# Optimization experiments

Hardware: AMD Instinct MI355X
Metric: run time of the kernel (lower is better)

Reference implementation:

```python
import jax, jax.numpy as jnp
import numpy as np

B = 8192
DIM = 1024
NI = 16
ALPHA = 0.5
BETA = 1.0


def setup_inputs() -> dict:
    key = jax.random.key(0)
    ks = jax.random.split(key, 12)
    d, n = DIM, NI
    din = d + d // n  # local expert input width = 1088
    s = 0.02  # small init scale to keep softplus in a sane range
    return {
        "y": jax.random.normal(ks[0], (B, d), jnp.float32),
        "M": jax.random.normal(ks[1], (B, d), jnp.float32),
        # global discriminator params ([in, out] layout)
        "gw0": jax.random.normal(ks[2], (d, d), jnp.float32) * s,
        "gb0": jnp.zeros((d,), jnp.float32),
        "gw1": jax.random.normal(ks[3], (d, d), jnp.float32) * s,
        "gb1": jnp.zeros((d,), jnp.float32),
        "l0w": jax.random.normal(ks[4], (2 * d, 128), jnp.float32) * s,
        "l0b": jnp.zeros((128,), jnp.float32),
        "l1w": jax.random.normal(ks[5], (128, 128), jnp.float32) * s,
        "l1b": jnp.zeros((128,), jnp.float32),
        "l2w": jax.random.normal(ks[6], (128, 1), jnp.float32) * s,
        "l2b": jnp.zeros((1,), jnp.float32),
        # local discriminator: n_interpretator stacked expert MLPs
        "lW1": jax.random.normal(ks[7], (n, din, 128), jnp.float32) * s,
        "lb1": jnp.zeros((n, 128), jnp.float32),
        "lW2": jax.random.normal(ks[8], (n, 128, 128), jnp.float32) * s,
        "lb2": jnp.zeros((n, 128), jnp.float32),
        "lW3": jax.random.normal(ks[9], (n, 128, 1), jnp.float32) * s,
        "lb3": jnp.zeros((n, 1), jnp.float32),
        "n_interpretator": NI,
    }


def reference(y, M, gw0, gb0, gw1, gb1, l0w, l0b, l1w, l1b, l2w, l2b,
              lW1, lb1, lW2, lb2, lW3, lb3, n_interpretator):
    n = n_interpretator
    Bsz, d = y.shape
    M3 = M.reshape(Bsz, d // n, n)                              # [B, d/n, n]
    Mp3 = jnp.concatenate([M3[1:], M3[:1]], axis=0)             # shuffled negatives
    y_exp = jnp.broadcast_to(y[:, :, None], (Bsz, d, n))        # [B, d, n]
    yM = jnp.concatenate([M3, y_exp], axis=1)                   # [B, d/n + d, n]
    yMp = jnp.concatenate([Mp3, y_exp], axis=1)

    def local_d(x):
        # batched over the n expert groups: grouped GEMMs instead of a loop
        h = jax.nn.relu(jnp.einsum('bdn,ndh->bnh', x, lW1) + lb1)   # [B, n, 128]
        h = jax.nn.relu(jnp.einsum('bnh,nhk->bnk', h, lW2) + lb2)   # [B, n, 128]
        s = jnp.einsum('bnh,nho->bno', h, lW3) + lb3                # [B, n, 1]
        return s[..., 0]                                            # [B, n]

    Ej_l = -jnp.mean(jax.nn.softplus(-local_d(yM)))
    Em_l = jnp.mean(jax.nn.softplus(local_d(yMp)))
    LOCAL = (Em_l - Ej_l) * BETA

    def global_d(yy, Mm):
        h = jax.nn.relu(Mm.reshape(Bsz, -1) @ gw0 + gb0) @ gw1 + gb1  # net(M)
        h = jnp.concatenate([yy, h], axis=1)                          # [B, 2d]
        h = jax.nn.relu(h @ l0w + l0b)
        h = jax.nn.relu(h @ l1w + l1b)
        return h @ l2w + l2b                                          # [B, 1]

    Ej_g = -jnp.mean(jax.nn.softplus(-global_d(y, M3)))
    Em_g = jnp.mean(jax.nn.softplus(global_d(y, Mp3)))
    GLOBAL = (Em_g - Ej_g) * ALPHA

    return LOCAL + GLOBAL
```

## Files before the change

kernel.cpp:

```cpp
#include <hip/hip_runtime.h>
#include <hip/hip_bf16.h>
#include <math.h>

#define B_ROWS 8192
#define NEXP 16

typedef __attribute__((ext_vector_type(8))) short short8;
typedef __attribute__((ext_vector_type(4))) float f32x4;

__device__ __forceinline__ float softplus_f(float x) {
    return fmaxf(x, 0.f) + log1pf(expf(-fabsf(x)));
}

__device__ __forceinline__ float bf2f(short u) {
    union { unsigned int i; float f; } c;
    c.i = ((unsigned int)(unsigned short)u) << 16;
    return c.f;
}

__device__ __forceinline__ short f2bf_s(float x) {
    __hip_bfloat16 h = __float2bfloat16(x);
    return *(short*)&h;
}

__device__ __forceinline__ void gll16(const void* g, void* l) {
    __builtin_amdgcn_global_load_lds(
        (const __attribute__((address_space(1))) void*)g,
        (__attribute__((address_space(3))) void*)l, 16, 0, 0);
}

#define FENCE() asm volatile("" ::: "memory")
#define VM3 asm volatile("s_waitcnt vmcnt(3)" ::: "memory")
#define VM0 asm volatile("s_waitcnt vmcnt(0)" ::: "memory")
#define BAR __builtin_amdgcn_s_barrier()

__global__ __launch_bounds__(256) void prep_all(
    const float* __restrict__ y, const float* __restrict__ M,
    const float* __restrict__ lW1, const float* __restrict__ gw0,
    const float* __restrict__ l0w, const float* __restrict__ gb1,
    const float* __restrict__ l0b, const float* __restrict__ lW2,
    const float* __restrict__ l1w, const float* __restrict__ gw1,
    __hip_bfloat16* __restrict__ yb, short* __restrict__ Mt2,
    __hip_bfloat16* __restrict__ W1yt, short* __restrict__ W1m2,
    __hip_bfloat16* __restrict__ W0p, __hip_bfloat16* __restrict__ l0wyt,
    float* __restrict__ bing, short* __restrict__ W2sb,
    short* __restrict__ L1ws, float* __restrict__ wgtp,
    double* __restrict__ acc, int* __restrict__ counter)
{
    __shared__ __align__(16) char smem[33280];
    const int b = blockIdx.x;
    const int tid = threadIdx.x;
    const int lane = tid & 63, w = tid >> 6;

    if (b < 64) {
        short* As = (short*)smem;
        short* Bs = (short*)(smem + 16384);
        const int ct = b & 7, ks = b >> 3;
        const int bn = ct * 128;
        const int wr = w >> 1, wc = w & 1;
        const int l15 = lane & 15, l4 = lane >> 4;

        f32x4 acc4[4][4] = {};
        for (int kq = 0; kq < 2; ++kq) {
            const int k0 = ks * 128 + kq * 64;
            {
                int c4 = (tid & 31) * 4;
                int kkr0 = tid >> 5;
                #pragma unroll
                for (int r = 0; r < 8; ++r) {
                    int kk = r * 8 + kkr0;
                    float4 v = *(const float4*)&l0w[(long)(1024 + k0 + kk) * 128 + c4];
                    int g = kk >> 3, sub = kk & 7;
                    #pragma unroll
                    for (int i = 0; i < 4; ++i) {
                        int row = c4 + i;
                        As[row * 64 + (g ^ (row & 7)) * 8 + sub] = f2bf_s(((const float*)&v)[i]);
                    }
                }
            }
            {
                int jr0 = tid >> 3;
                int g = tid & 7;
                #pragma unroll
                for (int s = 0; s < 4; ++s) {
                    int jrel = s * 32 + jr0;
                    const float* src = &gw1[(long)(bn + jrel) * 1024 + k0 + g * 8];
                    float4 v0 = *(const float4*)src;
                    float4 v1 = *(const float4*)(src + 4);
                    union { short8 v; short sh[8]; } o;
                    o.sh[0] = f2bf_s(v0.x); o.sh[1] = f2bf_s(v0.y);
                    o.sh[2] = f2bf_s(v0.z); o.sh[3] = f2bf_s(v0.w);
                    o.sh[4] = f2bf_s(v1.x); o.sh[5] = f2bf_s(v1.y);
                    o.sh[6] = f2bf_s(v1.z); o.sh[7] = f2bf_s(v1.w);
                    *(short8*)&Bs[jrel * 64 + (g ^ (jrel & 7)) * 8] = o.v;
                }
            }
            __syncthreads();
            #pragma unroll
            for (int st = 0; st < 2; ++st) {
                const int gr = (st * 4 + l4) ^ (l15 & 7);
                short8 a[4], bv[4];
                #pragma unroll
                for (int m = 0; m < 4; ++m)
                    a[m] = *(const short8*)&As[(wr * 64 + m * 16 + l15) * 64 + gr * 8];
                #pragma unroll
                for (int n = 0; n < 4; ++n)
                    bv[n] = *(const short8*)&Bs[(wc * 64 + n * 16 + l15) * 64 + gr * 8];
                #pragma unroll
                for (int m = 0; m < 4; ++m)
                    #pragma unroll
                    for (int n = 0; n < 4; ++n)
                        acc4[m][n] = __builtin_amdgcn_mfma_f32_16x16x32_bf16(a[m], bv[n], acc4[m][n], 0, 0, 0);
            }
            __syncthreads();
        }
        #pragma unroll
        for (int m = 0; m < 4; ++m) {
            int row = wr * 64 + m * 16 + l4 * 4;
            #pragma unroll
            for (int n = 0; n < 4; ++n) {
                int col = bn + wc * 64 + n * 16 + l15;
                #pragma unroll
                for (int r = 0; r < 4; ++r)
                    wgtp[((long)ks * 128 + row + r) * 1024 + col] = acc4[m][n][r];
            }
        }
        return;
    }

    if (b == 64) {
        float* part = (float*)smem;
        const int c = tid & 127, h2 = tid >> 7;
        float s = h2 ? 0.f : l0b[c];
        const float* p = l0w + (long)(1024 + h2 * 512) * 128 + c;
        const float* g = gb1 + h2 * 512;
        #pragma unroll 8
        for (int o = 0; o < 512; ++o)
            s = fmaf(g[o], p[(long)o * 128], s);
        part[tid] = s;
        __syncthreads();
        if (tid < 128) bing[tid] = part[tid] + part[tid + 128];
        if (tid == 255) { acc[0] = 0.0; acc[1] = 0.0; *counter = 0; }
        return;
    }

    if (b < 1089) {
        const long base = (long)(b - 65) * 2048;
        #pragma unroll
        for (int j = 0; j < 8; ++j) {
            long i = base + j * 256 + tid;
            float4 v = ((const float4*)y)[i];
            union { ushort4 u; __hip_bfloat16 h[4]; } p;
            p.h[0] = __float2bfloat16(v.x);
            p.h[1] = __float2bfloat16(v.y);
            p.h[2] = __float2bfloat16(v.z);
            p.h[3] = __float2bfloat16(v.w);
            ((ushort4*)yb)[i] = p.u;
        }
        return;
    }

    if (b < 2113) {
        short* t = (short*)smem;
        const long r0 = (long)(b - 1089) * 8;
        #pragma unroll
        for (int i = 0; i < 8; ++i) {
            int idx = i * 1024 + tid * 4;
            float4 v = *(const float4*)&M[r0 * 1024 + idx];
            short4 s;
            s.x = f2bf_s(v.x); s.y = f2bf_s(v.y); s.z = f2bf_s(v.z); s.w = f2bf_s(v.w);
            *(short4*)&t[idx] = s;
        }
        __syncthreads();
        const int e = tid & 15, rr = (tid >> 4) & 7, hf = tid >> 7;
        #pragma unroll
        for (int c = 0; c < 4; ++c) {
            union { short8 v; short s[8]; } o;
            #pragma unroll
            for (int j = 0; j < 8; ++j)
                o.s[j] = t[rr * 1024 + (hf * 32 + c * 8 + j) * 16 + e];
            *(short8*)&Mt2[(long)(e >> 1) * (8192L * 128) + (r0 + rr) * 128
                           + (e & 1) * 64 + hf * 32 + c * 8] = o.v;
        }
        return;
    }

    float (*t)[129] = (float(*)[129])smem;

    if (b < 2625) {
        int l = b - 2113, bx = l & 15, by = l >> 4;
        int n0 = bx * 128, k0 = by * 32;
        long base = 64L * 128 + (long)bx * (1088L * 128);
        #pragma unroll
        for (int ll = 0; ll < 16; ++ll) {
            int idx = tid + ll * 256;
            int kk = idx >> 7, nn = idx & 127;
            t[kk][nn] = lW1[base + (long)(k0 + kk) * 128 + nn];
        }
        __syncthreads();
        int nn = tid >> 1, kb = (tid & 1) * 16;
        #pragma unroll
        for (int j = 0; j < 16; ++j)
            W1yt[(long)(n0 + nn) * 1024 + k0 + kb + j] = __float2bfloat16(t[kb + j][nn]);
        return;
    }

    if (b < 2657) {
        int l = b - 2625, bx = l & 15, by = l >> 4;
        int n0 = bx * 128, k0 = by * 32;
        long base = (long)bx * (1088L * 128);
        #pragma unroll
        for (int ll = 0; ll < 16; ++ll) {
            int idx = tid + ll * 256;
            int kk = idx >> 7, nn = idx & 127;
            if (kk < 32) t[kk][nn] = lW1[base + (long)(k0 + kk) * 128 + nn];
        }
        __syncthreads();
        int nn = tid >> 1, kb = (tid & 1) * 16;
        int half = bx & 1;
        #pragma unroll
        for (int j = 0; j < 16; ++j) {
            W1m2[(long)(n0 + nn) * 128 + half * 64 + k0 + kb + j] = f2bf_s(t[kb + j][nn]);
            W1m2[(long)(n0 + nn) * 128 + (1 - half) * 64 + k0 + kb + j] = 0;
        }
        return;
    }

    if (b < 2913) {
        int l = b - 2657, bx = l & 7, by = l >> 3;
        int n0 = bx * 128, k0 = by * 32;
        int e = k0 >> 6, dd0 = k0 & 63;
        #pragma unroll
        for (int ll = 0; ll < 16; ++ll) {
            int idx = tid + ll * 256;
            int kk = idx >> 7, nn = idx & 127;
            t[kk][nn] = gw0[(long)((dd0 + kk) * 16 + e) * 1024 + n0 + nn];
        }
        __syncthreads();
        int nn = tid >> 1, kb = (tid & 1) * 16;
        #pragma unroll
        for (int j = 0; j < 16; ++j)
            W0p[(long)(n0 + nn) * 1024 + k0 + kb + j] = __float2bfloat16(t[kb + j][nn]);
        return;
    }

    if (b < 2945) {
        int by = b - 2913;
        int k0 = by * 32;
        #pragma unroll
        for (int ll = 0; ll < 16; ++ll) {
            int idx = tid + ll * 256;
            int kk = idx >> 7, nn = idx & 127;
            t[kk][nn] = l0w[(long)(k0 + kk) * 128 + nn];
        }
        __syncthreads();
        int nn = tid >> 1, kb = (tid & 1) * 16;
        #pragma unroll
        for (int j = 0; j < 16; ++j)
            l0wyt[(long)nn * 1024 + k0 + kb + j] = __float2bfloat16(t[kb + j][nn]);
        return;
    }

    {
        int bb = b - 2945;
        const float* in = (bb < 16) ? lW2 + (long)bb * 16384 : l1w;
        short* out = (bb < 16) ? W2sb + (long)bb * 16384 : L1ws;
        float (*t2)[65] = (float(*)[65])smem;
        #pragma unroll
        for (int h = 0; h < 2; ++h) {
            if (h) __syncthreads();
            #pragma unroll
            for (int l = 0; l < 32; ++l) {
                int idx = l * 256 + tid;
                int kk = idx >> 6, cc = idx & 63;
                t2[kk][cc] = in[(long)kk * 128 + h * 64 + cc];
            }
            __syncthreads();
            #pragma unroll
            for (int l = 0; l < 4; ++l) {
                int c2 = l * 256 + tid;
                int col = h * 64 + (c2 >> 4), kc = c2 & 15;
                int kcs = kc ^ (col & 7);
                union { short8 v; short s[8]; } u;
                #pragma unroll
                for (int j = 0; j < 8; ++j)
                    u.s[j] = f2bf_s(t2[kc * 8 + j][col - h * 64]);
                *(short8*)&out[col * 128 + kcs * 8] = u.v;
            }
        }
    }
}

__global__ __launch_bounds__(512, 4) void gemm3s(
    const short* __restrict__ yb, const short* __restrict__ W1yt,
    __hip_bfloat16* __restrict__ Y1b,
    const short* __restrict__ Mt2, const short* __restrict__ W1m2,
    __hip_bfloat16* __restrict__ Mpb,
    const short* __restrict__ W0p, const float* __restrict__ gb0,
    __hip_bfloat16* __restrict__ H0b,
    const float* __restrict__ wgtp, __hip_bfloat16* __restrict__ WgTb)
{
    __shared__ __align__(16) char smem[73728];
    const int tid = threadIdx.x;
    const int lane = tid & 63, w = tid >> 6;
    const int l15 = lane & 15, l4 = lane >> 4;
    const int wr = w >> 2, wc = w & 3;

    const int bid = blockIdx.x;

    if (bid >= 1280) {
        const int rb = bid - 1280;
        #pragma unroll
        for (int j = 0; j < 8; ++j) {
            int i4 = tid + j * 512;
            int flat = i4 * 4;
            int row = flat >> 7, cc = flat & 127;
            const long base = (long)row * 1024 + rb * 128 + cc;
            f32x4 s = {};
            #pragma unroll
            for (int ks = 0; ks < 8; ++ks) {
                f32x4 v = *(const f32x4*)&wgtp[(long)ks * 131072 + base];
                s += v;
            }
            union { ushort4 u; __hip_bfloat16 h[4]; } o;
            o.h[0] = __float2bfloat16(s[0]);
            o.h[1] = __float2bfloat16(s[1]);
            o.h[2] = __float2bfloat16(s[2]);
            o.h[3] = __float2bfloat16(s[3]);
            *(ushort4*)&WgTb[base] = o.u;
        }
        return;
    }

    const int xcd = bid & 7;
    const int idx = bid >> 3;

    int grp, bm, bn, K;
    const short* A; const short* Wt; __hip_bfloat16* C; int ldc;
    if (idx < 64) {
        grp = 0; const int c = idx >> 3, r = idx & 7;
        bm = (xcd * 8 + r) * 128; bn = c * 256;
        A = yb; Wt = W1yt + (long)bn * 1024; K = 1024; C = Y1b; ldc = 2048;
    } else if (idx < 96) {
        int j = idx - 64; const int c = j >> 3, r = j & 7;
        grp = 2; bm = (xcd * 8 + r) * 128; bn = c * 256;
        A = Mt2; Wt = W0p + (long)bn * 1024; K = 1024; C = H0b; ldc = 1024;
    } else {
        int j = idx - 96; const int c = j >> 3, r = j & 7;
        grp = 1; bm = (xcd * 8 + r) * 128; bn = c * 256;
        A = Mt2 + (long)c * (8192L * 128);
        Wt = W1m2 + (long)bn * 128; K = 128; C = Mpb; ldc = 2048;
    }
    const int nt = K >> 5;

    const int rowA = tid >> 2;
    const int sgA  = (tid & 3) ^ ((rowA >> 1) & 3);
    const int rowB0 = tid >> 2;
    const int sgB0  = (tid & 3) ^ ((rowB0 >> 1) & 3);
    const int rowB1 = (tid + 512) >> 2;
    const int sgB1  = (tid & 3) ^ ((rowB1 >> 1) & 3);

    auto STAGE = [&](int t, int sl) {
        char* base = smem + sl * 24576;
        const short* asrc;
        if (grp == 2) {
            const int g = t * 4 + sgA;
            asrc = A + (long)(g >> 4) * (8192L * 128)
                     + (long)(bm + rowA) * 128 + (g & 15) * 8;
        } else {
            asrc = A + (long)(bm + rowA) * K + t * 32 + sgA * 8;
        }
        gll16(asrc, base + w * 1024);
        gll16(Wt + (long)rowB0 * K + t * 32 + sgB0 * 8,
              base + 8192 + w * 1024);
        gll16(Wt + (long)rowB1 * K + t * 32 + sgB1 * 8,
              base + 16384 + w * 1024);
    };

    f32x4 acc[4][4] = {};
    const int xr = (l4 ^ ((l15 >> 1) & 3)) * 16;
    const int aOff = (wr * 64 + l15) * 64 + xr;
    const int bOff = 8192 + (wc * 64 + l15) * 64 + xr;

    auto PHASE = [&](int sl, int tn, int sl2, int mode) {
        const char* base = smem + sl * 24576;
        short8 a_[4], b_[4];
        #pragma unroll
        for (int m = 0; m < 4; ++m)
            a_[m] = *(const short8*)(base + aOff + m * 1024);
        #pragma unroll
        for (int n = 0; n < 4; ++n)
            b_[n] = *(const short8*)(base + bOff + n * 1024);
        if (mode == 0) { STAGE(tn, sl2); VM3; }
        else if (mode == 1) { VM0; }
        FENCE(); BAR; FENCE();
        __builtin_amdgcn_s_setprio(1);
        #pragma unroll
        for (int m = 0; m < 4; ++m)
            #pragma unroll
            for (int n = 0; n < 4; ++n)
                acc[m][n] = __builtin_amdgcn_mfma_f32_16x16x32_bf16(
                    a_[m], b_[n], acc[m][n], 0, 0, 0);
        __builtin_amdgcn_s_setprio(0);
        FENCE(); BAR; FENCE();
    };

    STAGE(0, 0);
    STAGE(1, 1);
    VM3; FENCE(); BAR; FENCE();

    int sl = 0, sl2 = 2;
    for (int t = 0; t < nt - 2; ++t) {
        PHASE(sl, t + 2, sl2, 0);
        sl = (sl == 2) ? 0 : sl + 1;
        sl2 = (sl2 == 2) ? 0 : sl2 + 1;
    }
    PHASE(sl, 0, 0, 1);
    sl = (sl == 2) ? 0 : sl + 1;
    PHASE(sl, 0, 0, 2);

    #pragma unroll
    for (int m = 0; m < 4; ++m) {
        const int row = bm + wr * 64 + m * 16 + l4 * 4;
        #pragma unroll
        for (int n = 0; n < 4; ++n) {
            const int col = bn + wc * 64 + n * 16 + l15;
            const float bv = (grp == 2) ? gb0[col] : 0.f;
            #pragma unroll
            for (int r = 0; r < 4; ++r) {
                float v = acc[m][n][r] + bv;
                if (grp == 2) v = fmaxf(v, 0.f);
                C[(long)(row + r) * ldc + col] = __float2bfloat16(v);
            }
        }
    }
}

__global__ __launch_bounds__(256) void tail_plus(
    const __hip_bfloat16* __restrict__ Yp, const __hip_bfloat16* __restrict__ Mq,
    const float* __restrict__ bin, const short* __restrict__ W2s,
    const float* __restrict__ b2, const float* __restrict__ w3,
    const float* __restrict__ b3, double* __restrict__ acc,
    const short* __restrict__ H0b, const short* __restrict__ WgTb,
    __hip_bfloat16* __restrict__ Tgb,
    const short* __restrict__ ybs, const short* __restrict__ l0ws,
    __hip_bfloat16* __restrict__ Tyb)
{
    __shared__ __align__(16) char smem[35328];
    const int bid = blockIdx.x;
    const int tid = threadIdx.x;
    const int lane = tid & 63;
    const int l15 = lane & 15, l4 = lane >> 4;

    if (bid >= 2048) {
        const int sel = bid - 2048;
        const short* Ain = (sel < 64) ? H0b : ybs;
        const short* Bin = (sel < 64) ? WgTb : l0ws;
        __hip_bfloat16* Co = (sel < 64) ? Tgb : Tyb;
        short* As = (short*)smem;
        short* Bs = (short*)(smem + 16384);
        const int w = tid >> 6;
        const int wr = w >> 1, wc = w & 1;
        const int bm = (sel & 63) * 128;
        const int srow = lane >> 3;
        const int gsrc = (lane & 7) ^ srow;

        f32x4 a4[4][4] = {};
        for (int k0 = 0; k0 < 1024; k0 += 64) {
            #pragma unroll
            for (int s = 0; s < 4; ++s) {
                const int rrel = s * 32 + w * 8 + srow;
                gll16(Ain + (long)(bm + rrel) * 1024 + k0 + gsrc * 8,
                      As + (s * 32 + w * 8) * 64);
                gll16(Bin + (long)rrel * 1024 + k0 + gsrc * 8,
                      Bs + (s * 32 + w * 8) * 64);
            }
            __syncthreads();
            #pragma unroll
            for (int st = 0; st < 2; ++st) {
                const int gr = (st * 4 + l4) ^ (l15 & 7);
                short8 a[4], b[4];
                #pragma unroll
                for (int m = 0; m < 4; ++m)
                    a[m] = *(const short8*)&As[(wr * 64 + m * 16 + l15) * 64 + gr * 8];
                #pragma unroll
                for (int n = 0; n < 4; ++n)
                    b[n] = *(const short8*)&Bs[(wc * 64 + n * 16 + l15) * 64 + gr * 8];
                #pragma unroll
                for (int m = 0; m < 4; ++m)
                    #pragma unroll
                    for (int n = 0; n < 4; ++n)
                        a4[m][n] = __builtin_amdgcn_mfma_f32_16x16x32_bf16(a[m], b[n], a4[m][n], 0, 0, 0);
            }
            __syncthreads();
        }
        #pragma unroll
        for (int m = 0; m < 4; ++m) {
            int row = bm + (w >> 1) * 64 + m * 16 + l4 * 4;
            #pragma unroll
            for (int n = 0; n < 4; ++n) {
                int col = (w & 1) * 64 + n * 16 + l15;
                #pragma unroll
                for (int r = 0; r < 4; ++r)
                    Co[(long)(row + r) * 128 + col] = __float2bfloat16(a4[m][n][r]);
            }
        }
        return;
    }

    const int wkid = (bid & 7) * 256 + (bid >> 3);
    const int e = wkid & 15;
    const int b0 = (wkid >> 4) * 64;
    const int cbase = e * 128;
    const int wid = tid >> 6;
    const int side = wid >> 1;
    const int wr = wid & 1;
    const int widthIn = 2048;

    short* h1 = (short*)smem;
    float* bins = (float*)(smem + 32768);
    float* b2s  = (float*)(smem + 33280);
    float* w3s  = (float*)(smem + 33792);
    float* red  = (float*)(smem + 34304);

    const short* W2e = W2s + (long)e * 16384;
    if (tid < 128) {
        bins[tid] = bin[cbase + tid];
        b2s[tid]  = b2[cbase + tid];
        w3s[tid]  = w3[cbase + tid];
    }
    __syncthreads();

    const short* Ys = (const short*)Yp;
    const short* Ms = (const short*)Mq;
    #pragma unroll
    for (int c = 0; c < 4; ++c) {
        int chunk = c * 256 + tid;
        int row = chunk >> 4, kc = chunk & 15;
        short8 yv = *(const short8*)&Ys[(long)(b0 + row) * widthIn + cbase + kc * 8];
        float yf[8];
        #pragma unroll
        for (int j = 0; j < 8; ++j) yf[j] = bf2f(yv[j]) + bins[kc * 8 + j];
        int dst = row * 128 + (kc ^ (row & 7)) * 8;
        #pragma unroll
        for (int s = 0; s < 2; ++s) {
            int rowm = (b0 + row + s) & (B_ROWS - 1);
            short8 mv = *(const short8*)&Ms[(long)rowm * widthIn + cbase + kc * 8];
            union { short8 v; short sh[8]; } o;
            #pragma unroll
            for (int j = 0; j < 8; ++j)
                o.sh[j] = f2bf_s(fmaxf(yf[j] + bf2f(mv[j]), 0.f));
            *(short8*)&h1[s * 8192 + dst] = o.v;
        }
    }
    __syncthreads();

    f32x4 accv[2][8] = {};
    #pragma unroll
    for (int st = 0; st < 4; ++st) {
        short8 a[2], b[8];
        #pragma unroll
        for (int m = 0; m < 2; ++m) {
            int row = wr * 32 + m * 16 + l15;
            int ch = (st * 4 + l4) ^ (row & 7);
            a[m] = *(const short8*)&h1[side * 8192 + row * 128 + ch * 8];
        }
        #pragma unroll
        for (int n = 0; n < 8; ++n) {
            int col = n * 16 + l15;
            int ch = (st * 4 + l4) ^ (col & 7);
            b[n] = *(const short8*)&W2e[col * 128 + ch * 8];
        }
        #pragma unroll
        for (int m = 0; m < 2; ++m)
            #pragma unroll
            for (int n = 0; n < 8; ++n)
                accv[m][n] = __builtin_amdgcn_mfma_f32_16x16x32_bf16(a[m], b[n], accv[m][n], 0, 0, 0);
    }

    float p[2][4] = {};
    #pragma unroll
    for (int m = 0; m < 2; ++m)
        #pragma unroll
        for (int n = 0; n < 8; ++n) {
            int colL = n * 16 + l15;
            float bb = b2s[colL], ww = w3s[colL];
            #pragma unroll
            for (int r = 0; r < 4; ++r) {
                float h2 = fmaxf(accv[m][n][r] + bb, 0.f);
                p[m][r] = fmaf(h2, ww, p[m][r]);
            }
        }
    #pragma unroll
    for (int m = 0; m < 2; ++m)
        #pragma unroll
        for (int r = 0; r < 4; ++r)
            #pragma unroll
            for (int off = 1; off < 16; off <<= 1)
                p[m][r] += __shfl_xor(p[m][r], off, 64);

    float mysum = 0.f;
    if (l15 == 0) {
        float bb = b3[e];
        #pragma unroll
        for (int m = 0; m < 2; ++m)
            #pragma unroll
            for (int r = 0; r < 4; ++r) {
                float s = p[m][r] + bb;
                mysum += softplus_f(side ? s : -s);
            }
    }
    red[tid] = mysum;
    __syncthreads();
    for (int s2 = 128; s2 > 0; s2 >>= 1) {
        if (tid < s2) red[tid] += red[tid + s2];
        __syncthreads();
    }
    if (tid == 0) atomicAdd(acc, (double)red[0]);
}

__global__ __launch_bounds__(256) void tail_mfma(
    const __hip_bfloat16* __restrict__ Yp, const __hip_bfloat16* __restrict__ Mq,
    const float* __restrict__ bin,
    const short* __restrict__ W2s,
    const float* __restrict__ b2, const float* __restrict__ w3,
    const float* __restrict__ b3,
    int widthIn, double* __restrict__ acc, int* __restrict__ counter,
    float* __restrict__ out)
{
    const int b0 = blockIdx.x * 64;
    const int e = blockIdx.y;
    const int cbase = e * 128;
    const int tid = threadIdx.x;
    const int lane = tid & 63;
    const int wid = tid >> 6;
    const int side = wid >> 1;
    const int wr = wid & 1;

    __shared__ __align__(16) short h1[2 * 64 * 128];
    __shared__ __align__(16) short Bs[128 * 128];
    __shared__ float bins[128], b2s[128], w3s[128];
    __shared__ float red[256];

    const short* W2e = W2s + (long)e * 16384;
    #pragma unroll
    for (int l = 0; l < 8; ++l) {
        int cb = (l * 4 + wid) * 64;
        gll16(W2e + (long)(cb + lane) * 8, &Bs[cb * 8]);
    }
    if (tid < 128) {
        bins[tid] = bin[cbase + tid];
        b2s[tid]  = b2[cbase + tid];
        w3s[tid]  = w3[cbase + tid];
    }
    __syncthreads();

    const short* Ys = (const short*)Yp;
    const short* Ms = (const short*)Mq;
    #pragma unroll
    for (int c = 0; c < 4; ++c) {
        int chunk = c * 256 + tid;
        int row = chunk >> 4, kc = chunk & 15;
        short8 yv = *(const short8*)&Ys[(long)(b0 + row) * widthIn + cbase + kc * 8];
        float yf[8];
        #pragma unroll
        for (int j = 0; j < 8; ++j) yf[j] = bf2f(yv[j]) + bins[kc * 8 + j];
        int dst = row * 128 + (kc ^ (row & 7)) * 8;
        #pragma unroll
        for (int s = 0; s < 2; ++s) {
            int rowm = (b0 + row + s) & (B_ROWS - 1);
            short8 mv = *(const short8*)&Ms[(long)rowm * widthIn + cbase + kc * 8];
            union { short8 v; short sh[8]; } o;
            #pragma unroll
            for (int j = 0; j < 8; ++j)
                o.sh[j] = f2bf_s(fmaxf(yf[j] + bf2f(mv[j]), 0.f));
            *(short8*)&h1[s * 8192 + dst] = o.v;
        }
    }
    __syncthreads();

    const int l15 = lane & 15, l4 = lane >> 4;
    f32x4 accv[2][8] = {};
    #pragma unroll
    for (int st = 0; st < 4; ++st) {
        short8 a[2], b[8];
        #pragma unroll
        for (int m = 0; m < 2; ++m) {
            int row = wr * 32 + m * 16 + l15;
            int ch = (st * 4 + l4) ^ (row & 7);
            a[m] = *(const short8*)&h1[side * 8192 + row * 128 + ch * 8];
        }
        #pragma unroll
        for (int n = 0; n < 8; ++n) {
            int col = n * 16 + l15;
            int ch = (st * 4 + l4) ^ (col & 7);
            b[n] = *(const short8*)&Bs[col * 128 + ch * 8];
        }
        #pragma unroll
        for (int m = 0; m < 2; ++m)
            #pragma unroll
            for (int n = 0; n < 8; ++n)
                accv[m][n] = __builtin_amdgcn_mfma_f32_16x16x32_bf16(a[m], b[n], accv[m][n], 0, 0, 0);
    }

    float p[2][4] = {};
    #pragma unroll
    for (int m = 0; m < 2; ++m)
        #pragma unroll
        for (int n = 0; n < 8; ++n) {
            int colL = n * 16 + l15;
            float bb = b2s[colL], ww = w3s[colL];
            #pragma unroll
            for (int r = 0; r < 4; ++r) {
                float h2 = fmaxf(accv[m][n][r] + bb, 0.f);
                p[m][r] = fmaf(h2, ww, p[m][r]);
            }
        }
    #pragma unroll
    for (int m = 0; m < 2; ++m)
        #pragma unroll
        for (int r = 0; r < 4; ++r)
            #pragma unroll
            for (int off = 1; off < 16; off <<= 1)
                p[m][r] += __shfl_xor(p[m][r], off, 64);

    float mysum = 0.f;
    if (l15 == 0) {
        float bb = b3[e];
        #pragma unroll
        for (int m = 0; m < 2; ++m)
            #pragma unroll
            for (int r = 0; r < 4; ++r) {
                float s = p[m][r] + bb;
                mysum += softplus_f(side ? s : -s);
            }
    }
    red[tid] = mysum;
    __syncthreads();
    for (int s2 = 128; s2 > 0; s2 >>= 1) {
        if (tid < s2) red[tid] += red[tid + s2];
        __syncthreads();
    }
    if (tid == 0) {
        atomicAdd(acc + 1, (double)red[0]);
        __threadfence();
        int old = atomicAdd(counter, 1);
        if (old == (int)(gridDim.x * gridDim.y) - 1) {
            double a0 = atomicAdd(acc + 0, 0.0);
            double a1 = atomicAdd(acc + 1, 0.0);
            out[0] = (float)(a0 / (8192.0 * 16.0) + 0.5 * a1 / 8192.0);
        }
    }
}

extern "C" void kernel_launch(void* const* d_in, const int* in_sizes, int n_in,
                              void* d_out, int out_size, void* d_ws, size_t ws_size,
                              hipStream_t stream)
{
    const float* y   = (const float*)d_in[0];
    const float* M   = (const float*)d_in[1];
    const float* gw0 = (const float*)d_in[2];
    const float* gb0 = (const float*)d_in[3];
    const float* gw1 = (const float*)d_in[4];
    const float* gb1 = (const float*)d_in[5];
    const float* l0w = (const float*)d_in[6];
    const float* l0b = (const float*)d_in[7];
    const float* l1w = (const float*)d_in[8];
    const float* l1b = (const float*)d_in[9];
    const float* l2w = (const float*)d_in[10];
    const float* l2b = (const float*)d_in[11];
    const float* lW1 = (const float*)d_in[12];
    const float* lb1 = (const float*)d_in[13];
    const float* lW2 = (const float*)d_in[14];
    const float* lb2 = (const float*)d_in[15];
    const float* lW3 = (const float*)d_in[16];
    const float* lb3 = (const float*)d_in[17];

    char* w = (char*)d_ws;
    double* acc = (double*)w;
    int* counter = (int*)(w + 16);
    float* bing = (float*)(w + 256);
    const size_t MB = 1u << 20;
    __hip_bfloat16* Y1b  = (__hip_bfloat16*)(w + 4096);
    __hip_bfloat16* Mpb  = (__hip_bfloat16*)(w + 4096 + 32 * MB);
    __hip_bfloat16* H0b  = (__hip_bfloat16*)(w + 4096 + 64 * MB);
    short*          Mt2  = (short*)(w + 4096 + 80 * MB);
    __hip_bfloat16* yb   = (__hip_bfloat16*)(w + 4096 + 96 * MB);
    __hip_bfloat16* W1yt = (__hip_bfloat16*)(w + 4096 + 112 * MB);
    __hip_bfloat16* W0p  = (__hip_bfloat16*)(w + 4096 + 118 * MB);
    __hip_bfloat16* l0wyt = (__hip_bfloat16*)(w + 4096 + 120 * MB);
    short* W2sb = (short*)(w + 4096 + 120 * MB + 512 * 1024);
    short* L1ws = (short*)(w + 4096 + 121 * MB);
    __hip_bfloat16* WgTb = (__hip_bfloat16*)(w + 4096 + 121 * MB + 512 * 1024);
    short* W1m2 = (short*)(w + 4096 + 122 * MB);
    __hip_bfloat16* Tyb = (__hip_bfloat16*)(w + 4096 + 123 * MB);
    __hip_bfloat16* Tgb = (__hip_bfloat16*)(w + 4096 + 125 * MB);
    float* wgtp = (float*)(w + 4096 + 123 * MB);

    dim3 blk(256);

    prep_all<<<dim3(2962), blk, 0, stream>>>(
        y, M, lW1, gw0, l0w, gb1, l0b, lW2, l1w, gw1,
        yb, Mt2, W1yt, W1m2, W0p, l0wyt, bing, W2sb, L1ws, wgtp,
        acc, counter);

    gemm3s<<<dim3(1288), dim3(512), 0, stream>>>(
        (const short*)yb, (const short*)W1yt, Y1b,
        Mt2, W1m2, Mpb,
        (const short*)W0p, gb0, H0b,
        wgtp, WgTb);

    tail_plus<<<dim3(2176), blk, 0, stream>>>(
        Y1b, Mpb, lb1, W2sb, lb2, lW3, lb3, acc,
        (const short*)H0b, (const short*)WgTb, Tgb,
        (const short*)yb, (const short*)l0wyt, Tyb);

    tail_mfma<<<dim3(128, 1), blk, 0, stream>>>(
        Tyb, Tgb, bing, L1ws, l1b, l2w, l2b, 128, acc, counter,
        (float*)d_out);
}
```

Measured before the change: 176.3 us.

## Shrink gemm3s tiles to 128x128 with 256 threads, move small prep work into it

The main grouped GEMM kernel now uses 128x128 output tiles with 256 threads (4 waves) and 48KB LDS instead of 128x256 tiles with 512 threads. This doubles the grid and raises occupancy (launch bounds 256,3). The triple-buffer loop is unrolled by three so ring slots are compile-time constants, and the wait count changes to match four loads per stage. The bias-fold, accumulator-reset and W2/L1 weight-swizzle blocks move from the prep kernel into the GEMM launch as extra blocks, so they can overlap with the GEMM. Smaller tiles reduce B-operand reuse per block and increase global traffic.

```diff
diff --git a/kernel.cpp b/kernel.cpp
--- a/kernel.cpp
+++ b/kernel.cpp
@@ -30,22 +30,18 @@
 }
 
 #define FENCE() asm volatile("" ::: "memory")
-#define VM3 asm volatile("s_waitcnt vmcnt(3)" ::: "memory")
+#define VM4 asm volatile("s_waitcnt vmcnt(4)" ::: "memory")
 #define VM0 asm volatile("s_waitcnt vmcnt(0)" ::: "memory")
 #define BAR __builtin_amdgcn_s_barrier()
 
 __global__ __launch_bounds__(256) void prep_all(
     const float* __restrict__ y, const float* __restrict__ M,
     const float* __restrict__ lW1, const float* __restrict__ gw0,
-    const float* __restrict__ l0w, const float* __restrict__ gb1,
-    const float* __restrict__ l0b, const float* __restrict__ lW2,
-    const float* __restrict__ l1w, const float* __restrict__ gw1,
+    const float* __restrict__ l0w, const float* __restrict__ gw1,
     __hip_bfloat16* __restrict__ yb, short* __restrict__ Mt2,
     __hip_bfloat16* __restrict__ W1yt, short* __restrict__ W1m2,
     __hip_bfloat16* __restrict__ W0p, __hip_bfloat16* __restrict__ l0wyt,
-    float* __restrict__ bing, short* __restrict__ W2sb,
-    short* __restrict__ L1ws, float* __restrict__ wgtp,
-    double* __restrict__ acc, int* __restrict__ counter)
+    float* __restrict__ wgtp)
 {
     __shared__ __align__(16) char smem[33280];
     const int b = blockIdx.x;
@@ -128,24 +124,8 @@
         return;
     }
 
-    if (b == 64) {
-        float* part = (float*)smem;
-        const int c = tid & 127, h2 = tid >> 7;
-        float s = h2 ? 0.f : l0b[c];
-        const float* p = l0w + (long)(1024 + h2 * 512) * 128 + c;
-        const float* g = gb1 + h2 * 512;
-        #pragma unroll 8
-        for (int o = 0; o < 512; ++o)
-            s = fmaf(g[o], p[(long)o * 128], s);
-        part[tid] = s;
-        __syncthreads();
-        if (tid < 128) bing[tid] = part[tid] + part[tid + 128];
-        if (tid == 255) { acc[0] = 0.0; acc[1] = 0.0; *counter = 0; }
-        return;
-    }
-
-    if (b < 1089) {
-        const long base = (long)(b - 65) * 2048;
+    if (b < 1088) {
+        const long base = (long)(b - 64) * 2048;
         #pragma unroll
         for (int j = 0; j < 8; ++j) {
             long i = base + j * 256 + tid;
@@ -160,9 +140,9 @@
         return;
     }
 
-    if (b < 2113) {
+    if (b < 2112) {
         short* t = (short*)smem;
-        const long r0 = (long)(b - 1089) * 8;
+        const long r0 = (long)(b - 1088) * 8;
         #pragma unroll
         for (int i = 0; i < 8; ++i) {
             int idx = i * 1024 + tid * 4;
@@ -187,8 +167,8 @@
 
     float (*t)[129] = (float(*)[129])smem;
 
-    if (b < 2625) {
-        int l = b - 2113, bx = l & 15, by = l >> 4;
+    if (b < 2624) {
+        int l = b - 2112, bx = l & 15, by = l >> 4;
         int n0 = bx * 128, k0 = by * 32;
         long base = 64L * 128 + (long)bx * (1088L * 128);
         #pragma unroll
@@ -205,8 +185,8 @@
         return;
     }
 
-    if (b < 2657) {
-        int l = b - 2625, bx = l & 15, by = l >> 4;
+    if (b < 2656) {
+        int l = b - 2624, bx = l & 15, by = l >> 4;
         int n0 = bx * 128, k0 = by * 32;
         long base = (long)bx * (1088L * 128);
         #pragma unroll
@@ -226,8 +206,8 @@
         return;
     }
 
-    if (b < 2913) {
-        int l = b - 2657, bx = l & 7, by = l >> 3;
+    if (b < 2912) {
+        int l = b - 2656, bx = l & 7, by = l >> 3;
         int n0 = bx * 128, k0 = by * 32;
         int e = k0 >> 6, dd0 = k0 & 63;
         #pragma unroll
@@ -244,8 +224,8 @@
         return;
     }
 
-    if (b < 2945) {
-        int by = b - 2913;
+    {
+        int by = b - 2912;
         int k0 = by * 32;
         #pragma unroll
         for (int ll = 0; ll < 16; ++ll) {
@@ -260,76 +240,98 @@
             l0wyt[(long)nn * 1024 + k0 + kb + j] = __float2bfloat16(t[kb + j][nn]);
         return;
     }
-
-    {
-        int bb = b - 2945;
-        const float* in = (bb < 16) ? lW2 + (long)bb * 16384 : l1w;
-        short* out = (bb < 16) ? W2sb + (long)bb * 16384 : L1ws;
-        float (*t2)[65] = (float(*)[65])smem;
-        #pragma unroll
-        for (int h = 0; h < 2; ++h) {
-            if (h) __syncthreads();
-            #pragma unroll
-            for (int l = 0; l < 32; ++l) {
-                int idx = l * 256 + tid;
-                int kk = idx >> 6, cc = idx & 63;
-                t2[kk][cc] = in[(long)kk * 128 + h * 64 + cc];
-            }
-            __syncthreads();
-            #pragma unroll
-            for (int l = 0; l < 4; ++l) {
-                int c2 = l * 256 + tid;
-                int col = h * 64 + (c2 >> 4), kc = c2 & 15;
-                int kcs = kc ^ (col & 7);
-                union { short8 v; short s[8]; } u;
-                #pragma unroll
-                for (int j = 0; j < 8; ++j)
-                    u.s[j] = f2bf_s(t2[kc * 8 + j][col - h * 64]);
-                *(short8*)&out[col * 128 + kcs * 8] = u.v;
-            }
-        }
-    }
 }
 
-__global__ __launch_bounds__(512, 4) void gemm3s(
+__global__ __launch_bounds__(256, 3) void gemm3s(
     const short* __restrict__ yb, const short* __restrict__ W1yt,
     __hip_bfloat16* __restrict__ Y1b,
     const short* __restrict__ Mt2, const short* __restrict__ W1m2,
     __hip_bfloat16* __restrict__ Mpb,
     const short* __restrict__ W0p, const float* __restrict__ gb0,
     __hip_bfloat16* __restrict__ H0b,
-    const float* __restrict__ wgtp, __hip_bfloat16* __restrict__ WgTb)
+    const float* __restrict__ wgtp, __hip_bfloat16* __restrict__ WgTb,
+    const float* __restrict__ l0w, const float* __restrict__ l0b,
+    const float* __restrict__ gb1, const float* __restrict__ lW2,
+    const float* __restrict__ l1w, float* __restrict__ bing,
+    short* __restrict__ W2sb, short* __restrict__ L1ws,
+    double* __restrict__ acc_g, int* __restrict__ counter)
 {
-    __shared__ __align__(16) char smem[73728];
+    __shared__ __align__(16) char smem[49152];
     const int tid = threadIdx.x;
     const int lane = tid & 63, w = tid >> 6;
     const int l15 = lane & 15, l4 = lane >> 4;
-    const int wr = w >> 2, wc = w & 3;
+    const int wr = w >> 1, wc = w & 1;
 
     const int bid = blockIdx.x;
 
-    if (bid >= 1280) {
-        const int rb = bid - 1280;
-        #pragma unroll
-        for (int j = 0; j < 8; ++j) {
-            int i4 = tid + j * 512;
-            int flat = i4 * 4;
-            int row = flat >> 7, cc = flat & 127;
-            const long base = (long)row * 1024 + rb * 128 + cc;
-            f32x4 s = {};
-            #pragma unroll
-            for (int ks = 0; ks < 8; ++ks) {
-                f32x4 v = *(const f32x4*)&wgtp[(long)ks * 131072 + base];
-                s += v;
-            }
-            union { ushort4 u; __hip_bfloat16 h[4]; } o;
-            o.h[0] = __float2bfloat16(s[0]);
-            o.h[1] = __float2bfloat16(s[1]);
-            o.h[2] = __float2bfloat16(s[2]);
-            o.h[3] = __float2bfloat16(s[3]);
-            *(ushort4*)&WgTb[base] = o.u;
-        }
-        return;
+    if (bid >= 2560) {
+        if (bid < 2568) {
+            const int rb = bid - 2560;
+            #pragma unroll
+            for (int j = 0; j < 16; ++j) {
+                int i4 = tid + j * 256;
+                int flat = i4 * 4;
+                int row = flat >> 7, cc = flat & 127;
+                const long base = (long)row * 1024 + rb * 128 + cc;
+                f32x4 s = {};
+                #pragma unroll
+                for (int ks = 0; ks < 8; ++ks) {
+                    f32x4 v = *(const f32x4*)&wgtp[(long)ks * 131072 + base];
+                    s += v;
+                }
+                union { ushort4 u; __hip_bfloat16 h[4]; } o;
+                o.h[0] = __float2bfloat16(s[0]);
+                o.h[1] = __float2bfloat16(s[1]);
+                o.h[2] = __float2bfloat16(s[2]);
+                o.h[3] = __float2bfloat16(s[3]);
+                *(ushort4*)&WgTb[base] = o.u;
+            }
+            return;
+        }
+        if (bid == 2568) {
+            float* part = (float*)smem;
+            const int c = tid & 127, h2 = tid >> 7;
+            float s = h2 ? 0.f : l0b[c];
+            const float* p = l0w + (long)(1024 + h2 * 512) * 128 + c;
+            const float* g = gb1 + h2 * 512;
+            #pragma unroll 8
+            for (int o = 0; o < 512; ++o)
+                s = fmaf(g[o], p[(long)o * 128], s);
+            part[tid] = s;
+            __syncthreads();
+            if (tid < 128) bing[tid] = part[tid] + part[tid + 128];
+            if (tid == 255) { acc_g[0] = 0.0; acc_g[1] = 0.0; *counter = 0; }
+            return;
+        }
+        {
+            int bb = bid - 2569;
+            const float* in = (bb < 16) ? lW2 + (long)bb * 16384 : l1w;
+            short* out = (bb < 16) ? W2sb + (long)bb * 16384 : L1ws;
+            float (*t2)[65] = (float(*)[65])smem;
+            #pragma unroll
+            for (int h = 0; h < 2; ++h) {
+                if (h) __syncthreads();
+                #pragma unroll
+                for (int l = 0; l < 32; ++l) {
+                    int idx = l * 256 + tid;
+                    int kk = idx >> 6, cc = idx & 63;
+                    t2[kk][cc] = in[(long)kk * 128 + h * 64 + cc];
+                }
+                __syncthreads();
+                #pragma unroll
+                for (int l = 0; l < 4; ++l) {
+                    int c2 = l * 256 + tid;
+                    int col = h * 64 + (c2 >> 4), kc = c2 & 15;
+                    int kcs = kc ^ (col & 7);
+                    union { short8 v; short s[8]; } u;
+                    #pragma unroll
+                    for (int j = 0; j < 8; ++j)
+                        u.s[j] = f2bf_s(t2[kc * 8 + j][col - h * 64]);
+                    *(short8*)&out[col * 128 + kcs * 8] = u.v;
+                }
+            }
+            return;
+        }
     }
 
     const int xcd = bid & 7;
@@ -337,44 +339,41 @@
 
     int grp, bm, bn, K;
     const short* A; const short* Wt; __hip_bfloat16* C; int ldc;
-    if (idx < 64) {
+    if (idx < 128) {
         grp = 0; const int c = idx >> 3, r = idx & 7;
-        bm = (xcd * 8 + r) * 128; bn = c * 256;
+        bm = (xcd * 8 + r) * 128; bn = c * 128;
         A = yb; Wt = W1yt + (long)bn * 1024; K = 1024; C = Y1b; ldc = 2048;
-    } else if (idx < 96) {
-        int j = idx - 64; const int c = j >> 3, r = j & 7;
-        grp = 2; bm = (xcd * 8 + r) * 128; bn = c * 256;
+    } else if (idx < 192) {
+        int j = idx - 128; const int c = j >> 3, r = j & 7;
+        grp = 2; bm = (xcd * 8 + r) * 128; bn = c * 128;
         A = Mt2; Wt = W0p + (long)bn * 1024; K = 1024; C = H0b; ldc = 1024;
     } else {
-        int j = idx - 96; const int c = j >> 3, r = j & 7;
-        grp = 1; bm = (xcd * 8 + r) * 128; bn = c * 256;
-        A = Mt2 + (long)c * (8192L * 128);
+        int j = idx - 192; const int c = j >> 3, r = j & 7;
+        grp = 1; bm = (xcd * 8 + r) * 128; bn = c * 128;
+        A = Mt2 + (long)(bn >> 8) * (8192L * 128);
         Wt = W1m2 + (long)bn * 128; K = 128; C = Mpb; ldc = 2048;
     }
     const int nt = K >> 5;
 
-    const int rowA = tid >> 2;
-    const int sgA  = (tid & 3) ^ ((rowA >> 1) & 3);
-    const int rowB0 = tid >> 2;
-    const int sgB0  = (tid & 3) ^ ((rowB0 >> 1) & 3);
-    const int rowB1 = (tid + 512) >> 2;
-    const int sgB1  = (tid & 3) ^ ((rowB1 >> 1) & 3);
-
     auto STAGE = [&](int t, int sl) {
-        char* base = smem + sl * 24576;
-        const short* asrc;
-        if (grp == 2) {
-            const int g = t * 4 + sgA;
-            asrc = A + (long)(g >> 4) * (8192L * 128)
-                     + (long)(bm + rowA) * 128 + (g & 15) * 8;
-        } else {
-            asrc = A + (long)(bm + rowA) * K + t * 32 + sgA * 8;
-        }
-        gll16(asrc, base + w * 1024);
-        gll16(Wt + (long)rowB0 * K + t * 32 + sgB0 * 8,
-              base + 8192 + w * 1024);
-        gll16(Wt + (long)rowB1 * K + t * 32 + sgB1 * 8,
-              base + 16384 + w * 1024);
+        char* base = smem + sl * 16384;
+        #pragma unroll
+        for (int p = 0; p < 2; ++p) {
+            const int u = p * 256 + tid;
+            const int row = u >> 2;
+            const int sg = (tid & 3) ^ ((row >> 1) & 3);
+            const short* asrc;
+            if (grp == 2) {
+                const int g = t * 4 + sg;
+                asrc = A + (long)(g >> 4) * (8192L * 128)
+                         + (long)(bm + row) * 128 + (g & 15) * 8;
+            } else {
+                asrc = A + (long)(bm + row) * K + t * 32 + sg * 8;
+            }
+            gll16(asrc, base + p * 4096 + w * 1024);
+            gll16(Wt + (long)row * K + t * 32 + sg * 8,
+                  base + 8192 + p * 4096 + w * 1024);
+        }
     };
 
     f32x4 acc[4][4] = {};
@@ -383,7 +382,7 @@
     const int bOff = 8192 + (wc * 64 + l15) * 64 + xr;
 
     auto PHASE = [&](int sl, int tn, int sl2, int mode) {
-        const char* base = smem + sl * 24576;
+        const char* base = smem + sl * 16384;
         short8 a_[4], b_[4];
         #pragma unroll
         for (int m = 0; m < 4; ++m)
@@ -391,7 +390,7 @@
         #pragma unroll
         for (int n = 0; n < 4; ++n)
             b_[n] = *(const short8*)(base + bOff + n * 1024);
-        if (mode == 0) { STAGE(tn, sl2); VM3; }
+        if (mode == 0) { STAGE(tn, sl2); VM4; }
         else if (mode == 1) { VM0; }
         FENCE(); BAR; FENCE();
         __builtin_amdgcn_s_setprio(1);
@@ -407,13 +406,20 @@
 
     STAGE(0, 0);
     STAGE(1, 1);
-    VM3; FENCE(); BAR; FENCE();
-
-    int sl = 0, sl2 = 2;
-    for (int t = 0; t < nt - 2; ++t) {
+    VM4; FENCE(); BAR; FENCE();
+
+    const int ntri = (nt - 2) / 3;
+    int t = 0;
+    for (int i = 0; i < ntri; ++i, t += 3) {
+        PHASE(0, t + 2, 2, 0);
+        PHASE(1, t + 3, 0, 0);
+        PHASE(2, t + 4, 1, 0);
+    }
+    int sl = t % 3;
+    for (; t < nt - 2; ++t) {
+        const int sl2 = (sl == 0) ? 2 : sl - 1;
         PHASE(sl, t + 2, sl2, 0);
         sl = (sl == 2) ? 0 : sl + 1;
-        sl2 = (sl2 == 2) ? 0 : sl2 + 1;
     }
     PHASE(sl, 0, 0, 1);
     sl = (sl == 2) ? 0 : sl + 1;
@@ -799,16 +805,17 @@
 
     dim3 blk(256);
 
-    prep_all<<<dim3(2962), blk, 0, stream>>>(
-        y, M, lW1, gw0, l0w, gb1, l0b, lW2, l1w, gw1,
-        yb, Mt2, W1yt, W1m2, W0p, l0wyt, bing, W2sb, L1ws, wgtp,
-        acc, counter);
-
-    gemm3s<<<dim3(1288), dim3(512), 0, stream>>>(
+    prep_all<<<dim3(2944), blk, 0, stream>>>(
+        y, M, lW1, gw0, l0w, gw1,
+        yb, Mt2, W1yt, W1m2, W0p, l0wyt, wgtp);
+
+    gemm3s<<<dim3(2586), blk, 0, stream>>>(
         (const short*)yb, (const short*)W1yt, Y1b,
         Mt2, W1m2, Mpb,
         (const short*)W0p, gb0, H0b,
-        wgtp, WgTb);
+        wgtp, WgTb,
+        l0w, l0b, gb1, lW2, l1w, bing, W2sb, L1ws,
+        acc, counter);
 
     tail_plus<<<dim3(2176), blk, 0, stream>>>(
         Y1b, Mpb, lb1, W2sb, lb2, lW3, lb3, acc,
```

Result: slower. 185.7 us (+5.4%).
